# Optimization experiments

Hardware: AMD Instinct MI355X
Metric: run time of the kernel (lower is better)

The kernel has to match this reference:

```python
import jax, jax.numpy as jnp
import numpy as np

N_HEADS = 12


def setup_inputs() -> dict:
    key = jax.random.key(0)
    ks = jax.random.split(key, 13)
    B, N, D, H = 8, 1024, 768, N_HEADS
    s = 0.05  # keep logits numerically sane
    return {
        "x": jax.random.normal(ks[0], (B, N, D), jnp.float32),
        "wq": jax.random.normal(ks[1], (D, D), jnp.float32) * s,
        "bq": jax.random.normal(ks[2], (D,), jnp.float32) * s,
        "wk": jax.random.normal(ks[3], (D, D), jnp.float32) * s,
        "bk": jax.random.normal(ks[4], (D,), jnp.float32) * s,
        "wv": jax.random.normal(ks[5], (D, D), jnp.float32) * s,
        "bv": jax.random.normal(ks[6], (D,), jnp.float32) * s,
        "wo": jax.random.normal(ks[7], (D, D), jnp.float32) * s,
        "bo": jax.random.normal(ks[8], (D,), jnp.float32) * s,
        "th1_w": jax.random.normal(ks[9], (H, H), jnp.float32) * (1.0 / H ** 0.5),
        "th1_b": jax.random.normal(ks[10], (H,), jnp.float32) * s,
        "th2_w": jax.random.normal(ks[11], (H, H), jnp.float32) * (1.0 / H ** 0.5),
        "th2_b": jax.random.normal(ks[12], (H,), jnp.float32) * s,
    }


def reference(x, wq, bq, wk, bk, wv, bv, wo, bo, th1_w, th1_b, th2_w, th2_b):
    B, N, D = x.shape
    H = N_HEADS
    hd = D // H
    scale = hd ** -0.5
    # projections (torch Linear: x @ W.T + b), split into heads -> [B,H,N,hd]
    def split_heads(y):
        return y.reshape(B, N, H, hd).transpose(0, 2, 1, 3)
    q = split_heads(x @ wq.T + bq)
    k = split_heads(x @ wk.T + bk)
    v = split_heads(x @ wv.T + bv)
    # attention logits [B,H,N,N]
    attn = jnp.einsum("bhnd,bhmd->bhnm", q, k) * scale
    # talking-heads mix 1 (1x1 conv over head dim)
    attn = jnp.einsum("gh,bhnm->bgnm", th1_w, attn) + th1_b[None, :, None, None]
    attn = jax.nn.softmax(attn, axis=-1)
    # talking-heads mix 2
    attn = jnp.einsum("gh,bhnm->bgnm", th2_w, attn) + th2_b[None, :, None, None]
    # (dropout p=0.0 -> identity)
    out = jnp.einsum("bhnm,bhmd->bhnd", attn, v)  # [B,H,N,hd]
    out = out.transpose(0, 2, 1, 3).reshape(B, N, D)
    return out @ wo.T + bo
```

## Files before the change

### kernel.cpp

```cpp
#include <hip/hip_runtime.h>
#include <hip/hip_bf16.h>

typedef __attribute__((ext_vector_type(8))) short short8;
typedef __attribute__((ext_vector_type(4))) float f32x4;
typedef __attribute__((ext_vector_type(2))) float f32x2;
typedef __attribute__((ext_vector_type(4))) int i32x4;
typedef __attribute__((ext_vector_type(2))) int i32x2;

typedef unsigned short u16;
typedef unsigned int u32;

#define DEVI static __device__ __forceinline__

constexpr int Bn = 8, Nn = 1024, Dn = 768, Hn = 12;
constexpr int Rn = Bn * Nn;
constexpr int LDQ = 3 * Dn;
constexpr int KOFF = Dn, VOFF = 2 * Dn;
constexpr float SCALE = 0.125f;
constexpr float LOG2E = 1.44269504088896340736f;

DEVI size_t sidx(int bb, int n, int h) {
    return (((size_t)bb * Nn + n) * Hn + h) * Nn;
}

DEVI u16 f2bf(float f) {
    __hip_bfloat16 h = __float2bfloat16(f);
    return __builtin_bit_cast(u16, h);
}

DEVI u32 bfpack(float a, float b) {
    u32 xa = __builtin_bit_cast(u32, a);
    u32 xb = __builtin_bit_cast(u32, b);
    xa += 0x7fffu + ((xa >> 16) & 1u);
    xb += 0x7fffu + ((xb >> 16) & 1u);
    return (xa >> 16) | (xb & 0xffff0000u);
}

#if __has_builtin(__builtin_amdgcn_exp2f)
#define EXP2(x) __builtin_amdgcn_exp2f(x)
#else
#define EXP2(x) exp2f(x)
#endif
#if __has_builtin(__builtin_amdgcn_rcpf)
#define RCP(x) __builtin_amdgcn_rcpf(x)
#else
#define RCP(x) (1.0f / (x))
#endif

DEVI void gload16(const u16* g, u16* l) {
    __builtin_amdgcn_global_load_lds(
        (const __attribute__((address_space(1))) void*)g,
        (__attribute__((address_space(3))) void*)l,
        16, 0, 0);
}

__global__ __launch_bounds__(256) void cvt4_kernel(const float* __restrict__ in,
                                                   u16* __restrict__ out, int n4) {
    int i = blockIdx.x * 256 + threadIdx.x;
    if (i >= n4) return;
    f32x4 v = *reinterpret_cast<const f32x4*>(&in[(size_t)i * 4]);
    u16 o[4];
#pragma unroll
    for (int j = 0; j < 4; ++j) o[j] = f2bf(v[j]);
    *reinterpret_cast<u32*>(&out[(size_t)i * 4]) = (u32)o[0] | ((u32)o[1] << 16);
    *reinterpret_cast<u32*>(&out[(size_t)i * 4 + 2]) = (u32)o[2] | ((u32)o[3] << 16);
}

__global__ __launch_bounds__(256) void cvtw_kernel(const float* __restrict__ a,
                                                   const float* __restrict__ b,
                                                   const float* __restrict__ c,
                                                   const float* __restrict__ d,
                                                   u16* oa, u16* ob, u16* oc, u16* od,
                                                   int n4) {
    int i = blockIdx.x * 256 + threadIdx.x;
    if (i >= n4) return;
    const float* in; u16* out;
    switch (blockIdx.y) {
        case 0: in = a; out = oa; break;
        case 1: in = b; out = ob; break;
        case 2: in = c; out = oc; break;
        default: in = d; out = od; break;
    }
    f32x4 v = *reinterpret_cast<const f32x4*>(&in[(size_t)i * 4]);
    u16 o[4];
#pragma unroll
    for (int j = 0; j < 4; ++j) o[j] = f2bf(v[j]);
    *reinterpret_cast<u32*>(&out[(size_t)i * 4]) = (u32)o[0] | ((u32)o[1] << 16);
    *reinterpret_cast<u32*>(&out[(size_t)i * 4 + 2]) = (u32)o[2] | ((u32)o[3] << 16);
}

__global__ __launch_bounds__(256) void bcat_kernel(const float* __restrict__ a,
                                                   const float* __restrict__ b,
                                                   const float* __restrict__ c,
                                                   float* __restrict__ o) {
    int i = blockIdx.x * 256 + threadIdx.x;
    if (i < Dn) o[i] = a[i];
    else if (i < 2 * Dn) o[i] = b[i - Dn];
    else if (i < 3 * Dn) o[i] = c[i - 2 * Dn];
}

template <bool BF16OUT>
__global__ __launch_bounds__(256) void gemm128(const u16* __restrict__ A,
                                               const u16* __restrict__ Bm,
                                               const float* __restrict__ bias,
                                               void* __restrict__ Cv,
                                               int M, int Nc, int K) {
    __shared__ u16 lA[128 * 32];
    __shared__ u16 lB[128 * 32];
    int tid = threadIdx.x, wave = tid >> 6, lane = tid & 63;
    int wr = (wave >> 1) * 64, wc = (wave & 1) * 64;

    int nwg = gridDim.x * gridDim.y;
    int bid = blockIdx.y * gridDim.x + blockIdx.x;
    if ((nwg & 7) == 0) {
        int cpx = nwg >> 3;
        bid = (bid & 7) * cpx + (bid >> 3);
    }
    int row0 = (bid / gridDim.x) * 128, col0 = (bid % gridDim.x) * 128;

    f32x4 acc[4][4] = {};

    int sseg = (tid & 3) ^ ((tid >> 3) & 3);
    const u16* gA = A + (size_t)(row0 + (tid >> 2)) * K + sseg * 8;
    const u16* gB = Bm + (size_t)(col0 + (tid >> 2)) * K + sseg * 8;
    u16* sA = &lA[tid * 8];
    u16* sB = &lB[tid * 8];

    int sw8 = (((lane >> 4) ^ ((lane >> 1) & 3))) * 8;

    for (int k0 = 0; k0 < K; k0 += 32) {
        gload16(gA + k0, sA);
        gload16(gA + k0 + (size_t)64 * K, sA + 2048);
        gload16(gB + k0, sB);
        gload16(gB + k0 + (size_t)64 * K, sB + 2048);
        __syncthreads();

        short8 af[4], bf[4];
#pragma unroll
        for (int a = 0; a < 4; ++a)
            af[a] = *reinterpret_cast<const short8*>(
                &lA[(wr + a * 16 + (lane & 15)) * 32 + sw8]);
#pragma unroll
        for (int c = 0; c < 4; ++c)
            bf[c] = *reinterpret_cast<const short8*>(
                &lB[(wc + c * 16 + (lane & 15)) * 32 + sw8]);
#pragma unroll
        for (int a = 0; a < 4; ++a)
#pragma unroll
            for (int c = 0; c < 4; ++c)
                acc[a][c] = __builtin_amdgcn_mfma_f32_16x16x32_bf16(af[a], bf[c], acc[a][c], 0, 0, 0);
        __syncthreads();
    }

#pragma unroll
    for (int a = 0; a < 4; ++a) {
        int crow = row0 + wr + a * 16 + (lane >> 4) * 4;
#pragma unroll
        for (int c = 0; c < 4; ++c) {
            int col = col0 + wc + c * 16 + (lane & 15);
            float bv = bias ? bias[col] : 0.f;
#pragma unroll
            for (int r = 0; r < 4; ++r) {
                float v = acc[a][c][r] + bv;
                if (BF16OUT)
                    reinterpret_cast<u16*>(Cv)[(size_t)(crow + r) * Nc + col] = f2bf(v);
                else
                    reinterpret_cast<float*>(Cv)[(size_t)(crow + r) * Nc + col] = v;
            }
        }
    }
}

__global__ __launch_bounds__(256) void qk_kernel(const u16* __restrict__ QKV,
                                                 u16* __restrict__ S, int b0) {
    __shared__ u16 lQ[64 * 64];
    __shared__ u16 lK[64 * 64];
    int z = blockIdx.z, h = z % Hn, bb = z / Hn, b = b0 + bb;
    int n0 = blockIdx.y * 64, m0 = blockIdx.x * 64;
    int tid = threadIdx.x, wave = tid >> 6, lane = tid & 63;

    int srow = tid >> 3;
    int s8 = (tid & 7) ^ (srow & 7);
    const u16* gQ = QKV + ((size_t)(b * Nn) + n0 + srow) * LDQ + h * 64 + s8 * 8;
    const u16* gK = QKV + ((size_t)(b * Nn) + m0 + srow) * LDQ + KOFF + h * 64 + s8 * 8;
    gload16(gQ, &lQ[tid * 8]);
    gload16(gQ + (size_t)32 * LDQ, &lQ[tid * 8 + 2048]);
    gload16(gK, &lK[tid * 8]);
    gload16(gK + (size_t)32 * LDQ, &lK[tid * 8 + 2048]);
    __syncthreads();

    f32x4 acc[4] = {};
#pragma unroll
    for (int kk = 0; kk < 2; ++kk) {
        int ko = kk * 4 + (lane >> 4);
        int sw = (ko ^ (lane & 7)) * 8;
        short8 bf = *reinterpret_cast<const short8*>(
            &lK[(wave * 16 + (lane & 15)) * 64 + sw]);
#pragma unroll
        for (int a = 0; a < 4; ++a) {
            short8 af = *reinterpret_cast<const short8*>(
                &lQ[(a * 16 + (lane & 15)) * 64 + sw]);
            acc[a] = __builtin_amdgcn_mfma_f32_16x16x32_bf16(af, bf, acc[a], 0, 0, 0);
        }
    }

    int col = m0 + wave * 16 + (lane & 15);
#pragma unroll
    for (int a = 0; a < 4; ++a) {
        int rowb = n0 + a * 16 + (lane >> 4) * 4;
#pragma unroll
        for (int r = 0; r < 4; ++r)
            S[sidx(bb, rowb + r, h) + col] = f2bf(acc[a][r] * SCALE);
    }
}

__global__ __launch_bounds__(256) void mid_kernel(u16* __restrict__ S,
                                                  const float* __restrict__ w1p,
                                                  const float* __restrict__ b1p,
                                                  const float* __restrict__ w2p,
                                                  const float* __restrict__ b2p) {
    __shared__ float w1[Hn * Hn], w2[Hn * Hn], b1v[Hn], b2v[Hn];
    __shared__ float redS[4][Hn];
    int tid = threadIdx.x;
    for (int i = tid; i < Hn * Hn; i += 256) {
        int g = i % Hn, h = i / Hn;
        w1[i] = w1p[g * Hn + h] * LOG2E;
        w2[i] = w2p[g * Hn + h];
    }
    if (tid < Hn) { b1v[tid] = b1p[tid] * LOG2E; b2v[tid] = b2p[tid]; }
    __syncthreads();

    int bb = blockIdx.x >> 10, n = blockIdx.x & 1023;
    size_t base0 = sidx(bb, n, 0) + tid * 4;

    i32x2 sv[Hn];
#pragma unroll
    for (int h = 0; h < Hn; ++h)
        sv[h] = *reinterpret_cast<const i32x2*>(&S[base0 + h * Nn]);

    f32x2 acc[Hn][2];
#pragma unroll
    for (int g = 0; g < Hn; ++g) {
        float b = b1v[g];
        acc[g][0] = f32x2{b, b};
        acc[g][1] = f32x2{b, b};
    }

#pragma unroll
    for (int h = 0; h < Hn; ++h) {
        u32 u0 = (u32)sv[h][0], u1 = (u32)sv[h][1];
        f32x2 v0, v1;
        v0[0] = __builtin_bit_cast(float, u0 << 16);
        v0[1] = __builtin_bit_cast(float, u0 & 0xffff0000u);
        v1[0] = __builtin_bit_cast(float, u1 << 16);
        v1[1] = __builtin_bit_cast(float, u1 & 0xffff0000u);
#pragma unroll
        for (int g = 0; g < Hn; ++g) {
            float w = w1[h * Hn + g];
            f32x2 wv = {w, w};
            acc[g][0] += wv * v0;
            acc[g][1] += wv * v1;
        }
    }

    float sm[Hn];
#pragma unroll
    for (int g = 0; g < Hn; ++g) {
        acc[g][0][0] = EXP2(acc[g][0][0]);
        acc[g][0][1] = EXP2(acc[g][0][1]);
        acc[g][1][0] = EXP2(acc[g][1][0]);
        acc[g][1][1] = EXP2(acc[g][1][1]);
        f32x2 s2 = acc[g][0] + acc[g][1];
        sm[g] = s2[0] + s2[1];
    }
#pragma unroll
    for (int off = 32; off; off >>= 1)
#pragma unroll
        for (int g = 0; g < Hn; ++g) sm[g] += __shfl_xor(sm[g], off, 64);
    int wv2 = tid >> 6, ln = tid & 63;
    if (ln < Hn) redS[wv2][ln] = sm[ln];
    __syncthreads();
#pragma unroll
    for (int g = 0; g < Hn; ++g) {
        float inv = RCP(redS[0][g] + redS[1][g] + redS[2][g] + redS[3][g]);
        f32x2 iv = {inv, inv};
        acc[g][0] *= iv;
        acc[g][1] *= iv;
    }

#pragma unroll
    for (int g = 0; g < Hn; ++g) {
        float b = b2v[g];
        f32x2 o0 = {b, b}, o1 = {b, b};
#pragma unroll
        for (int h = 0; h < Hn; ++h) {
            float w = w2[h * Hn + g];
            f32x2 wv = {w, w};
            o0 += wv * acc[h][0];
            o1 += wv * acc[h][1];
        }
        i32x2 ob;
        ob[0] = (int)bfpack(o0[0], o0[1]);
        ob[1] = (int)bfpack(o1[0], o1[1]);
        *reinterpret_cast<i32x2*>(&S[base0 + g * Nn]) = ob;
    }
}

__global__ __launch_bounds__(256) void vtrans_kernel(const u16* __restrict__ QKV,
                                                     u16* __restrict__ Vt) {
    __shared__ u16 lT[64 * 64];
    int bg = blockIdx.y, g = bg % Hn, b = bg / Hn;
    int m0 = blockIdx.x * 64;
    int tid = threadIdx.x;

    int r = tid >> 3, d8 = tid & 7;
#pragma unroll
    for (int p = 0; p < 2; ++p) {
        int rr = r + p * 32;
        i32x4 v = *reinterpret_cast<const i32x4*>(
            &QKV[((size_t)(b * Nn) + m0 + rr) * LDQ + VOFF + g * 64 + d8 * 8]);
        *reinterpret_cast<i32x4*>(&lT[rr * 64 + ((d8 ^ (rr & 7)) * 8)]) = v;
    }
    __syncthreads();

    int d = tid >> 3, rs = (tid & 7) * 8;
#pragma unroll
    for (int p = 0; p < 2; ++p) {
        int dd = d + p * 32;
        u16 o[8];
#pragma unroll
        for (int j = 0; j < 8; ++j)
            o[j] = lT[(rs + j) * 64 + (((dd >> 3) ^ j) * 8) + (dd & 7)];
        *reinterpret_cast<i32x4*>(&Vt[((size_t)(b * Hn + g) * 64 + dd) * Nn + m0 + rs]) =
            *reinterpret_cast<const i32x4*>(o);
    }
}

__global__ __launch_bounds__(256) void pv_kernel(const u16* __restrict__ S,
                                                 const u16* __restrict__ Vt,
                                                 u16* __restrict__ O, int b0) {
    __shared__ u16 lA[128 * 32];
    __shared__ u16 lB[64 * 32];
    int tid = threadIdx.x, wave = tid >> 6, lane = tid & 63;

    int nwg = gridDim.x * gridDim.y;
    int bid = blockIdx.y * gridDim.x + blockIdx.x;
    if ((nwg & 7) == 0) {
        int cpx = nwg >> 3;
        bid = (bid & 7) * cpx + (bid >> 3);
    }
    int zz = bid / gridDim.x, g = zz % Hn, bb = zz / Hn, b = b0 + bb;
    int n0 = (bid % gridDim.x) * 128;

    constexpr size_t RS = (size_t)Hn * Nn;
    f32x4 acc[2][4] = {};
    int sseg = (tid & 3) ^ ((tid >> 3) & 3);
    const u16* gA = S + sidx(bb, n0 + (tid >> 2), g) + sseg * 8;
    const u16* gB = Vt + ((size_t)(b * Hn + g) * 64 + (tid >> 2)) * Nn + sseg * 8;
    u16* sA = &lA[tid * 8];
    u16* sB = &lB[tid * 8];

    int sw8 = (((lane >> 4) ^ ((lane >> 1) & 3))) * 8;

    for (int m0 = 0; m0 < Nn; m0 += 32) {
        gload16(gA + m0, sA);
        gload16(gA + m0 + 64 * RS, sA + 2048);
        gload16(gB + m0, sB);
        __syncthreads();

        short8 bf[4];
#pragma unroll
        for (int c = 0; c < 4; ++c)
            bf[c] = *reinterpret_cast<const short8*>(
                &lB[(c * 16 + (lane & 15)) * 32 + sw8]);
#pragma unroll
        for (int a = 0; a < 2; ++a) {
            short8 af = *reinterpret_cast<const short8*>(
                &lA[(wave * 32 + a * 16 + (lane & 15)) * 32 + sw8]);
#pragma unroll
            for (int c = 0; c < 4; ++c)
                acc[a][c] = __builtin_amdgcn_mfma_f32_16x16x32_bf16(af, bf[c], acc[a][c], 0, 0, 0);
        }
        __syncthreads();
    }

#pragma unroll
    for (int a = 0; a < 2; ++a) {
        int orow = n0 + wave * 32 + a * 16 + (lane >> 4) * 4;
#pragma unroll
        for (int c = 0; c < 4; ++c) {
            int ocol = g * 64 + c * 16 + (lane & 15);
#pragma unroll
            for (int r = 0; r < 4; ++r)
                O[((size_t)(b * Nn) + orow + r) * Dn + ocol] = f2bf(acc[a][c][r]);
        }
    }
}

extern "C" void kernel_launch(void* const* d_in, const int* in_sizes, int n_in,
                              void* d_out, int out_size, void* d_ws, size_t ws_size,
                              hipStream_t stream) {
    const float* x    = (const float*)d_in[0];
    const float* wq   = (const float*)d_in[1];
    const float* bq   = (const float*)d_in[2];
    const float* wk   = (const float*)d_in[3];
    const float* bk   = (const float*)d_in[4];
    const float* wv   = (const float*)d_in[5];
    const float* bv   = (const float*)d_in[6];
    const float* wo   = (const float*)d_in[7];
    const float* bo   = (const float*)d_in[8];
    const float* th1w = (const float*)d_in[9];
    const float* th1b = (const float*)d_in[10];
    const float* th2w = (const float*)d_in[11];
    const float* th2b = (const float*)d_in[12];

    size_t off = 0;
    auto alloc = [&](size_t bytes) {
        void* p = (char*)d_ws + off;
        off += (bytes + 255) & ~(size_t)255;
        return p;
    };
    const size_t RD2 = (size_t)Rn * Dn * 2;
    const size_t DD = (size_t)Dn * Dn;
    u16*   xb    = (u16*)alloc(RD2);
    u16*   qkvb  = (u16*)alloc((size_t)Rn * LDQ * 2);
    u16*   vtb   = (u16*)alloc(RD2);
    u16*   wqkvb = (u16*)alloc(3 * DD * 2);
    u16*   wob   = (u16*)alloc(DD * 2);
    float* bqkv  = (float*)alloc(3 * Dn * 4);

    const size_t SB = (size_t)Hn * Nn * Nn * 2;
    size_t base = off;
    int conc = 1;
    if (ws_size > base + SB) {
        size_t c = (ws_size - base) / SB;
        conc = c > 4 ? 4 : (int)c;
    }
    u16* sb = (u16*)((char*)d_ws + base);

    cvt4_kernel<<<(Rn * Dn / 4 + 255) / 256, 256, 0, stream>>>(x, xb, Rn * Dn / 4);
    cvtw_kernel<<<dim3((Dn * Dn / 4 + 255) / 256, 4), 256, 0, stream>>>(
        wq, wk, wv, wo, wqkvb, wqkvb + DD, wqkvb + 2 * DD, wob, Dn * Dn / 4);
    bcat_kernel<<<(3 * Dn + 255) / 256, 256, 0, stream>>>(bq, bk, bv, bqkv);

    gemm128<true><<<dim3(LDQ / 128, Rn / 128), 256, 0, stream>>>(
        xb, wqkvb, bqkv, qkvb, Rn, LDQ, Dn);

    vtrans_kernel<<<dim3(Nn / 64, Bn * Hn), 256, 0, stream>>>(qkvb, vtb);

    for (int b0 = 0; b0 < Bn; b0 += conc) {
        int g = (Bn - b0) < conc ? (Bn - b0) : conc;
        qk_kernel<<<dim3(Nn / 64, Nn / 64, Hn * g), 256, 0, stream>>>(qkvb, sb, b0);
        mid_kernel<<<g * Nn, 256, 0, stream>>>(sb, th1w, th1b, th2w, th2b);
        pv_kernel<<<dim3(Nn / 128, Hn * g), 256, 0, stream>>>(sb, vtb, xb, b0);
    }

    gemm128<false><<<dim3(Dn / 128, Rn / 128), 256, 0, stream>>>(
        xb, wob, bo, d_out, Rn, Dn, Dn);
}
```

Before: 292.1 us.

## Double-buffer LDS tiles in GEMM and PV kernels to overlap loads with MFMA

Both the projection GEMM and the PV kernel now keep two LDS buffers per operand. The next K-slice is issued into the alternate buffer before the MFMAs on the current slice run, so each iteration needs one barrier instead of two. This is meant to hide global-to-LDS load latency behind compute, at the cost of twice the shared memory per block, which may reduce occupancy. Correctness depends on gload16 writes to the other buffer not racing with reads, which the single trailing barrier is meant to cover.

```diff
diff --git a/kernel.cpp b/kernel.cpp
--- a/kernel.cpp
+++ b/kernel.cpp
@@ -105,8 +105,8 @@
                                                const float* __restrict__ bias,
                                                void* __restrict__ Cv,
                                                int M, int Nc, int K) {
-    __shared__ u16 lA[128 * 32];
-    __shared__ u16 lB[128 * 32];
+    __shared__ u16 lA[2][128 * 32];
+    __shared__ u16 lB[2][128 * 32];
     int tid = threadIdx.x, wave = tid >> 6, lane = tid & 63;
     int wr = (wave >> 1) * 64, wc = (wave & 1) * 64;
 
@@ -123,33 +123,41 @@
     int sseg = (tid & 3) ^ ((tid >> 3) & 3);
     const u16* gA = A + (size_t)(row0 + (tid >> 2)) * K + sseg * 8;
     const u16* gB = Bm + (size_t)(col0 + (tid >> 2)) * K + sseg * 8;
-    u16* sA = &lA[tid * 8];
-    u16* sB = &lB[tid * 8];
+
+    auto stage = [&](int buf, int k0) {
+        gload16(gA + k0, &lA[buf][tid * 8]);
+        gload16(gA + k0 + (size_t)64 * K, &lA[buf][tid * 8 + 2048]);
+        gload16(gB + k0, &lB[buf][tid * 8]);
+        gload16(gB + k0 + (size_t)64 * K, &lB[buf][tid * 8 + 2048]);
+    };
 
     int sw8 = (((lane >> 4) ^ ((lane >> 1) & 3))) * 8;
 
-    for (int k0 = 0; k0 < K; k0 += 32) {
-        gload16(gA + k0, sA);
-        gload16(gA + k0 + (size_t)64 * K, sA + 2048);
-        gload16(gB + k0, sB);
-        gload16(gB + k0 + (size_t)64 * K, sB + 2048);
-        __syncthreads();
+    int nt = K / 32;
+    stage(0, 0);
+    __syncthreads();
+
+    int cur = 0;
+    for (int t = 0; t < nt; ++t) {
+        if (t + 1 < nt) stage(cur ^ 1, (t + 1) * 32);
 
         short8 af[4], bf[4];
 #pragma unroll
         for (int a = 0; a < 4; ++a)
             af[a] = *reinterpret_cast<const short8*>(
-                &lA[(wr + a * 16 + (lane & 15)) * 32 + sw8]);
+                &lA[cur][(wr + a * 16 + (lane & 15)) * 32 + sw8]);
 #pragma unroll
         for (int c = 0; c < 4; ++c)
             bf[c] = *reinterpret_cast<const short8*>(
-                &lB[(wc + c * 16 + (lane & 15)) * 32 + sw8]);
+                &lB[cur][(wc + c * 16 + (lane & 15)) * 32 + sw8]);
 #pragma unroll
         for (int a = 0; a < 4; ++a)
 #pragma unroll
             for (int c = 0; c < 4; ++c)
                 acc[a][c] = __builtin_amdgcn_mfma_f32_16x16x32_bf16(af[a], bf[c], acc[a][c], 0, 0, 0);
+
         __syncthreads();
+        cur ^= 1;
     }
 
 #pragma unroll
@@ -339,8 +347,8 @@
 __global__ __launch_bounds__(256) void pv_kernel(const u16* __restrict__ S,
                                                  const u16* __restrict__ Vt,
                                                  u16* __restrict__ O, int b0) {
-    __shared__ u16 lA[128 * 32];
-    __shared__ u16 lB[64 * 32];
+    __shared__ u16 lA[2][128 * 32];
+    __shared__ u16 lB[2][64 * 32];
     int tid = threadIdx.x, wave = tid >> 6, lane = tid & 63;
 
     int nwg = gridDim.x * gridDim.y;
@@ -357,31 +365,38 @@
     int sseg = (tid & 3) ^ ((tid >> 3) & 3);
     const u16* gA = S + sidx(bb, n0 + (tid >> 2), g) + sseg * 8;
     const u16* gB = Vt + ((size_t)(b * Hn + g) * 64 + (tid >> 2)) * Nn + sseg * 8;
-    u16* sA = &lA[tid * 8];
-    u16* sB = &lB[tid * 8];
+
+    auto stage = [&](int buf, int m0) {
+        gload16(gA + m0, &lA[buf][tid * 8]);
+        gload16(gA + m0 + 64 * RS, &lA[buf][tid * 8 + 2048]);
+        gload16(gB + m0, &lB[buf][tid * 8]);
+    };
 
     int sw8 = (((lane >> 4) ^ ((lane >> 1) & 3))) * 8;
 
-    for (int m0 = 0; m0 < Nn; m0 += 32) {
-        gload16(gA + m0, sA);
-        gload16(gA + m0 + 64 * RS, sA + 2048);
-        gload16(gB + m0, sB);
-        __syncthreads();
+    stage(0, 0);
+    __syncthreads();
+
+    int cur = 0;
+    for (int t = 0; t < Nn / 32; ++t) {
+        if (t + 1 < Nn / 32) stage(cur ^ 1, (t + 1) * 32);
 
         short8 bf[4];
 #pragma unroll
         for (int c = 0; c < 4; ++c)
             bf[c] = *reinterpret_cast<const short8*>(
-                &lB[(c * 16 + (lane & 15)) * 32 + sw8]);
+                &lB[cur][(c * 16 + (lane & 15)) * 32 + sw8]);
 #pragma unroll
         for (int a = 0; a < 2; ++a) {
             short8 af = *reinterpret_cast<const short8*>(
-                &lA[(wave * 32 + a * 16 + (lane & 15)) * 32 + sw8]);
+                &lA[cur][(wave * 32 + a * 16 + (lane & 15)) * 32 + sw8]);
 #pragma unroll
             for (int c = 0; c < 4; ++c)
                 acc[a][c] = __builtin_amdgcn_mfma_f32_16x16x32_bf16(af, bf[c], acc[a][c], 0, 0, 0);
         }
+
         __syncthreads();
+        cur ^= 1;
     }
 
 #pragma unroll
```

Result: slower. 300.1 us (+2.8%).
